# Kernel optimization log

Measured on AMD Instinct MI355X. Metric: run time of the kernel, lower is better.

## Reference

```python
import jax, jax.numpy as jnp
import numpy as np

V = 30522   # vocab / node count
A = 2       # num adjacency matrices
H = 128     # hid_dim
O = 16      # out_dim
B = 8       # batch
D = 256     # doc/sequence dim
NNZ = 250000  # nonzeros per adjacency


def setup_inputs() -> dict:
    key = jax.random.key(0)
    k = jax.random.split(key, 7)
    x_dv = jax.random.normal(k[0], (B, D, V), jnp.float32)
    adj_rows = jax.random.randint(k[1], (A, NNZ), 0, V)
    adj_cols = jax.random.randint(k[2], (A, NNZ), 0, V)
    adj_vals = jax.random.uniform(k[3], (A, NNZ), jnp.float32)
    W_vh = jax.random.normal(k[4], (A, V, H), jnp.float32) * 0.02
    fc_W = jax.random.normal(k[5], (H, O), jnp.float32) * 0.05
    fc_b = jnp.zeros((O,), jnp.float32)
    return {"x_dv": x_dv, "adj_rows": adj_rows, "adj_cols": adj_cols,
            "adj_vals": adj_vals, "W_vh": W_vh, "fc_W": fc_W, "fc_b": fc_b}


def reference(x_dv, adj_rows, adj_cols, adj_vals, W_vh, fc_W, fc_b):
    # Per-adjacency sparse mm: h_vh[a] = A_a @ W_a, A_a in COO form. [A, V, H]
    def spmm(rows, cols, vals, W):
        # gather rows of W at cols, scale by vals, scatter-add into output rows
        return jax.ops.segment_sum(vals[:, None] * W[cols], rows, num_segments=V)

    h_vh = jax.vmap(spmm)(adj_rows, adj_cols, adj_vals, W_vh)  # [A, V, H]
    # Dropout is identity in eval mode. fused_h = sum_a x_dv @ h_vh[a]
    # = x_dv @ sum_a h_vh[a] (x_dv is shared across adjacencies).
    h_sum = h_vh.sum(axis=0)                                   # [V, H]
    fused_h = jnp.einsum('bdv,vh->bdh', x_dv, h_sum)           # [B, D, H]
    return fused_h @ fc_W + fc_b                               # [B, D, O]
```

## Files before the change

### kernel.cpp

```cpp
#include <hip/hip_runtime.h>

#define V_N 30522
#define A_N 2
#define H_N 128
#define O_N 16
#define NNZ_N 250000
#define NNZ_T (A_N * NNZ_N)
#define M_N 2048
#define AV_N (A_N * V_N)

#define KPAD 30720
#define KSPL 32
#define KC (KPAD / KSPL)
#define NCHUNK 30
#define PADW (KPAD - V_N)

typedef __attribute__((ext_vector_type(8))) short bf16x8_t;
typedef __attribute__((ext_vector_type(4))) float f32x4_t;

static __device__ __forceinline__ unsigned short f2bf(float f) {
    union { float f; unsigned u; } v; v.f = f;
    unsigned r = v.u + 0x7fffu + ((v.u >> 16) & 1u);
    return (unsigned short)(r >> 16);
}

__global__ __launch_bounds__(256) void wfc_kernel(const float* __restrict__ W,
                                                  const float* __restrict__ fcW,
                                                  float* __restrict__ wfc,
                                                  int* __restrict__ count) {
    int gtid = blockIdx.x * 256 + threadIdx.x;
    if (gtid < V_N) count[gtid] = 0;

    __shared__ float wrow[16][128];
    int row0 = blockIdx.x * 16;
    for (int idx = threadIdx.x; idx < 16 * 32; idx += 256) {
        int r = idx >> 5, c4 = (idx & 31) * 4;
        int grow = row0 + r;
        float4 v = make_float4(0.f, 0.f, 0.f, 0.f);
        if (grow < AV_N)
            v = *reinterpret_cast<const float4*>(W + (size_t)grow * H_N + c4);
        *reinterpret_cast<float4*>(&wrow[r][c4]) = v;
    }
    __syncthreads();
    int r = threadIdx.x >> 4, o = threadIdx.x & 15;
    int grow = row0 + r;
    if (grow >= AV_N) return;
    float s = 0.f;
#pragma unroll
    for (int h = 0; h < H_N; ++h) s += wrow[r][h] * fcW[h * O_N + o];
    wfc[(size_t)grow * O_N + o] = s;
}

__global__ __launch_bounds__(256) void hist_kernel(const int* __restrict__ rows,
                                                   int* __restrict__ count,
                                                   short* __restrict__ hw_t) {
    int n = blockIdx.x * blockDim.x + threadIdx.x;
    if (n < O_N * PADW) {
        int o = n / PADW, v2 = V_N + (n - o * PADW);
        hw_t[(size_t)o * KPAD + v2] = 0;
    }
    if (n >= NNZ_T) return;
    atomicAdd(&count[rows[n]], 1);
}

__global__ __launch_bounds__(1024) void scanA_kernel(const int* __restrict__ count,
                                                     int* __restrict__ csum) {
    __shared__ int sdata[1024];
    int tid = threadIdx.x;
    int i = blockIdx.x * 1024 + tid;
    sdata[tid] = (i < V_N) ? count[i] : 0;
    __syncthreads();
    for (int off = 512; off > 0; off >>= 1) {
        if (tid < off) sdata[tid] += sdata[tid + off];
        __syncthreads();
    }
    if (tid == 0) csum[blockIdx.x] = sdata[0];
}

__global__ __launch_bounds__(1024) void scanC_kernel(const int* __restrict__ count,
                                                     const int* __restrict__ csum,
                                                     int* __restrict__ row_start,
                                                     int* __restrict__ cursor) {
    __shared__ int sdata[1024];
    __shared__ int coff_s;
    int tid = threadIdx.x;
    int bid = blockIdx.x;
    if (tid < 32) {
        int own = (tid < NCHUNK) ? csum[tid] : 0;
        int v = own;
#pragma unroll
        for (int d = 1; d < 32; d <<= 1) {
            int t = __shfl_up(v, d, 32);
            if (tid >= d) v += t;
        }
        if (tid == bid) coff_s = v - own;
        if (bid == 0 && tid == NCHUNK - 1) row_start[V_N] = v;
    }
    int i = bid * 1024 + tid;
    int v = (i < V_N) ? count[i] : 0;
    sdata[tid] = v;
    __syncthreads();
    for (int off = 1; off < 1024; off <<= 1) {
        int t = (tid >= off) ? sdata[tid - off] : 0;
        __syncthreads();
        sdata[tid] += t;
        __syncthreads();
    }
    int exc = sdata[tid] - v + coff_s;
    if (i < V_N) { row_start[i] = exc; cursor[i] = exc; }
}

__global__ __launch_bounds__(256) void scatter_kernel(const int* __restrict__ rows,
                                                      const int* __restrict__ cols,
                                                      const float* __restrict__ vals,
                                                      int* __restrict__ cursor,
                                                      unsigned long long* __restrict__ scv) {
    int n = blockIdx.x * blockDim.x + threadIdx.x;
    if (n >= NNZ_T) return;
    int a = (n >= NNZ_N) ? 1 : 0;
    int r = rows[n];
    int pos = atomicAdd(&cursor[r], 1);
    union { float f; unsigned u; } uv; uv.f = vals[n];
    scv[pos] = ((unsigned long long)uv.u << 32) | (unsigned)(a * V_N + cols[n]);
}

__global__ __launch_bounds__(256) void accum_hw_kernel(const int* __restrict__ row_start,
                                                       const unsigned long long* __restrict__ scv,
                                                       const float* __restrict__ wfc,
                                                       short* __restrict__ hw_t) {
    int gid = blockIdx.x * blockDim.x + threadIdx.x;
    if (gid >= V_N * O_N) return;
    int row = gid >> 4, o = gid & 15;
    int s = row_start[row];
    int e = row_start[row + 1];
    float acc = 0.f;
    for (int i = s; i < e; ++i) {
        unsigned long long cv = scv[i];
        int cp = (int)(cv & 0xffffffffu);
        union { unsigned u; float f; } uv; uv.u = (unsigned)(cv >> 32);
        acc += uv.f * wfc[(size_t)cp * O_N + o];
    }
    hw_t[(size_t)o * KPAD + row] = (short)f2bf(acc);
}

__global__ __launch_bounds__(256) void gemm_mfma5(const float* __restrict__ X,
                                                  const short* __restrict__ hw_t,
                                                  float* __restrict__ partials) {
    const int tid = threadIdx.x;
    const int w = tid >> 6;
    const int lane = tid & 63;
    const int l15 = lane & 15;
    const int kg = lane >> 4;
    const int row0 = blockIdx.x * 64 + w * 16;
    const int by = blockIdx.y;
    const int k0 = by * KC;

    const float* xrow = X + (size_t)(row0 + l15) * V_N;
    const short* hrow = hw_t + (size_t)l15 * KPAD;

    f32x4_t acc = {};

#pragma unroll 2
    for (int kb = k0; kb < k0 + KC; kb += 32) {
        int k = kb + kg * 8;
        float a[8];
        if (k + 7 < V_N) {
            const float2* p = reinterpret_cast<const float2*>(xrow + k);
            float2 u0 = p[0], u1 = p[1], u2 = p[2], u3 = p[3];
            a[0] = u0.x; a[1] = u0.y; a[2] = u1.x; a[3] = u1.y;
            a[4] = u2.x; a[5] = u2.y; a[6] = u3.x; a[7] = u3.y;
        } else {
#pragma unroll
            for (int j = 0; j < 8; ++j) a[j] = (k + j < V_N) ? xrow[k + j] : 0.f;
        }
        bf16x8_t av;
#pragma unroll
        for (int j = 0; j < 8; ++j) av[j] = (short)f2bf(a[j]);
        bf16x8_t bv = *reinterpret_cast<const bf16x8_t*>(hrow + k);
        acc = __builtin_amdgcn_mfma_f32_16x16x32_bf16(av, bv, acc, 0, 0, 0);
    }

#pragma unroll
    for (int r4 = 0; r4 < 4; ++r4)
        partials[((size_t)by * M_N + row0 + kg * 4 + r4) * O_N + l15] = acc[r4];
}

__global__ __launch_bounds__(256) void reduce_kernel(const float* __restrict__ partials,
                                                     const float* __restrict__ fcb,
                                                     float* __restrict__ out) {
    int idx = blockIdx.x * 256 + threadIdx.x;
    if (idx >= M_N * O_N) return;
    float s = fcb[idx & 15];
#pragma unroll
    for (int by = 0; by < KSPL; ++by)
        s += partials[(size_t)by * M_N * O_N + idx];
    out[idx] = s;
}

extern "C" void kernel_launch(void* const* d_in, const int* in_sizes, int n_in,
                              void* d_out, int out_size, void* d_ws, size_t ws_size,
                              hipStream_t stream) {
    const float* x    = (const float*)d_in[0];
    const int* rows   = (const int*)d_in[1];
    const int* cols   = (const int*)d_in[2];
    const float* vals = (const float*)d_in[3];
    const float* W    = (const float*)d_in[4];
    const float* fcW  = (const float*)d_in[5];
    const float* fcb  = (const float*)d_in[6];
    float* out = (float*)d_out;

    char* base = (char*)d_ws;
    size_t off = 0;
    auto alloc = [&](size_t bytes) { size_t p = off; off = (off + bytes + 255) & ~(size_t)255; return p; };
    size_t o_wfc    = alloc((size_t)AV_N * O_N * 4);
    size_t o_hwt    = alloc((size_t)O_N * KPAD * 2);
    size_t o_count  = alloc((size_t)V_N * 4);
    size_t o_rstart = alloc((size_t)(V_N + 1) * 4);
    size_t o_cursor = alloc((size_t)V_N * 4);
    size_t o_scv    = alloc((size_t)NNZ_T * 8);
    size_t o_csum   = alloc((size_t)NCHUNK * 4);
    size_t o_part   = alloc((size_t)KSPL * M_N * O_N * 4);

    float* wfc        = (float*)(base + o_wfc);
    short* hw_t       = (short*)(base + o_hwt);
    int*   count      = (int*)(base + o_count);
    int*   row_start  = (int*)(base + o_rstart);
    int*   cursor     = (int*)(base + o_cursor);
    unsigned long long* scv = (unsigned long long*)(base + o_scv);
    int*   csum       = (int*)(base + o_csum);
    float* partials   = (float*)(base + o_part);

    wfc_kernel<<<(AV_N + 15) / 16, 256, 0, stream>>>(W, fcW, wfc, count);
    hist_kernel<<<(NNZ_T + 255) / 256, 256, 0, stream>>>(rows, count, hw_t);
    scanA_kernel<<<NCHUNK, 1024, 0, stream>>>(count, csum);
    scanC_kernel<<<NCHUNK, 1024, 0, stream>>>(count, csum, row_start, cursor);
    scatter_kernel<<<(NNZ_T + 255) / 256, 256, 0, stream>>>(rows, cols, vals, cursor, scv);
    accum_hw_kernel<<<(V_N * O_N + 255) / 256, 256, 0, stream>>>(row_start, scv, wfc, hw_t);

    gemm_mfma5<<<dim3(M_N / 64, KSPL), 256, 0, stream>>>(x, hw_t, partials);
    reduce_kernel<<<(M_N * O_N + 255) / 256, 256, 0, stream>>>(partials, fcb, out);
}
```

Before: 164.7 us.

## Pre-convert X to padded bf16 in quarters piggybacked on sparse-prep kernels

Each of the four sparse-preparation kernels now also converts a quarter of the fp32 input X into a padded bf16 buffer. The GEMM reads bf16 directly instead of loading fp32 and converting in its inner loop. The aim is to hide the X conversion behind the latency-bound sparse kernels and to halve the bytes the GEMM streams. In exchange, X is still read once as fp32, plus an extra bf16 write of about 126MB and a bf16 reread. The approach also depends on those small kernels having spare bandwidth.

New measurement: 206.8 us. 25.5% more time.

```diff
diff --git a/kernel.cpp b/kernel.cpp
--- a/kernel.cpp
+++ b/kernel.cpp
@@ -14,6 +14,9 @@
 #define KC (KPAD / KSPL)
 #define NCHUNK 30
 #define PADW (KPAD - V_N)
+#define KP8 (KPAD / 8)
+#define NCV (M_N * KP8)
+#define QCH (NCV / 4)
 
 typedef __attribute__((ext_vector_type(8))) short bf16x8_t;
 typedef __attribute__((ext_vector_type(4))) float f32x4_t;
@@ -24,10 +27,38 @@
     return (unsigned short)(r >> 16);
 }
 
+static __device__ __forceinline__ void convert_slice(const float* __restrict__ X,
+                                                     short* __restrict__ xb,
+                                                     int slice) {
+    const int end = (slice + 1) * QCH;
+    const int stride = gridDim.x * blockDim.x;
+    for (int c = slice * QCH + blockIdx.x * blockDim.x + threadIdx.x; c < end; c += stride) {
+        int m = c / KP8;
+        int k0 = (c - m * KP8) * 8;
+        const float* xr = X + (size_t)m * V_N + k0;
+        bf16x8_t o;
+        if (k0 + 7 < V_N) {
+            const float2* p = reinterpret_cast<const float2*>(xr);
+            float2 u0 = p[0], u1 = p[1], u2 = p[2], u3 = p[3];
+            o[0] = (short)f2bf(u0.x); o[1] = (short)f2bf(u0.y);
+            o[2] = (short)f2bf(u1.x); o[3] = (short)f2bf(u1.y);
+            o[4] = (short)f2bf(u2.x); o[5] = (short)f2bf(u2.y);
+            o[6] = (short)f2bf(u3.x); o[7] = (short)f2bf(u3.y);
+        } else {
+#pragma unroll
+            for (int j = 0; j < 8; ++j)
+                o[j] = (k0 + j < V_N) ? (short)f2bf(xr[j]) : (short)0;
+        }
+        *reinterpret_cast<bf16x8_t*>(xb + (size_t)m * KPAD + k0) = o;
+    }
+}
+
 __global__ __launch_bounds__(256) void wfc_kernel(const float* __restrict__ W,
                                                   const float* __restrict__ fcW,
                                                   float* __restrict__ wfc,
-                                                  int* __restrict__ count) {
+                                                  int* __restrict__ count,
+                                                  const float* __restrict__ X,
+                                                  short* __restrict__ xb) {
     int gtid = blockIdx.x * 256 + threadIdx.x;
     if (gtid < V_N) count[gtid] = 0;
 
@@ -44,23 +75,27 @@
     __syncthreads();
     int r = threadIdx.x >> 4, o = threadIdx.x & 15;
     int grow = row0 + r;
-    if (grow >= AV_N) return;
-    float s = 0.f;
-#pragma unroll
-    for (int h = 0; h < H_N; ++h) s += wrow[r][h] * fcW[h * O_N + o];
-    wfc[(size_t)grow * O_N + o] = s;
+    if (grow < AV_N) {
+        float s = 0.f;
+#pragma unroll
+        for (int h = 0; h < H_N; ++h) s += wrow[r][h] * fcW[h * O_N + o];
+        wfc[(size_t)grow * O_N + o] = s;
+    }
+    convert_slice(X, xb, 0);
 }
 
 __global__ __launch_bounds__(256) void hist_kernel(const int* __restrict__ rows,
                                                    int* __restrict__ count,
-                                                   short* __restrict__ hw_t) {
+                                                   short* __restrict__ hw_t,
+                                                   const float* __restrict__ X,
+                                                   short* __restrict__ xb) {
     int n = blockIdx.x * blockDim.x + threadIdx.x;
     if (n < O_N * PADW) {
         int o = n / PADW, v2 = V_N + (n - o * PADW);
         hw_t[(size_t)o * KPAD + v2] = 0;
     }
-    if (n >= NNZ_T) return;
-    atomicAdd(&count[rows[n]], 1);
+    if (n < NNZ_T) atomicAdd(&count[rows[n]], 1);
+    convert_slice(X, xb, 1);
 }
 
 __global__ __launch_bounds__(1024) void scanA_kernel(const int* __restrict__ count,
@@ -114,36 +149,44 @@
                                                       const int* __restrict__ cols,
                                                       const float* __restrict__ vals,
                                                       int* __restrict__ cursor,
-                                                      unsigned long long* __restrict__ scv) {
+                                                      unsigned long long* __restrict__ scv,
+                                                      const float* __restrict__ X,
+                                                      short* __restrict__ xb) {
     int n = blockIdx.x * blockDim.x + threadIdx.x;
-    if (n >= NNZ_T) return;
-    int a = (n >= NNZ_N) ? 1 : 0;
-    int r = rows[n];
-    int pos = atomicAdd(&cursor[r], 1);
-    union { float f; unsigned u; } uv; uv.f = vals[n];
-    scv[pos] = ((unsigned long long)uv.u << 32) | (unsigned)(a * V_N + cols[n]);
+    if (n < NNZ_T) {
+        int a = (n >= NNZ_N) ? 1 : 0;
+        int r = rows[n];
+        int pos = atomicAdd(&cursor[r], 1);
+        union { float f; unsigned u; } uv; uv.f = vals[n];
+        scv[pos] = ((unsigned long long)uv.u << 32) | (unsigned)(a * V_N + cols[n]);
+    }
+    convert_slice(X, xb, 2);
 }
 
 __global__ __launch_bounds__(256) void accum_hw_kernel(const int* __restrict__ row_start,
                                                        const unsigned long long* __restrict__ scv,
                                                        const float* __restrict__ wfc,
-                                                       short* __restrict__ hw_t) {
+                                                       short* __restrict__ hw_t,
+                                                       const float* __restrict__ X,
+                                                       short* __restrict__ xb) {
     int gid = blockIdx.x * blockDim.x + threadIdx.x;
-    if (gid >= V_N * O_N) return;
-    int row = gid >> 4, o = gid & 15;
-    int s = row_start[row];
-    int e = row_start[row + 1];
-    float acc = 0.f;
-    for (int i = s; i < e; ++i) {
-        unsigned long long cv = scv[i];
-        int cp = (int)(cv & 0xffffffffu);
-        union { unsigned u; float f; } uv; uv.u = (unsigned)(cv >> 32);
-        acc += uv.f * wfc[(size_t)cp * O_N + o];
-    }
-    hw_t[(size_t)o * KPAD + row] = (short)f2bf(acc);
-}
-
-__global__ __launch_bounds__(256) void gemm_mfma5(const float* __restrict__ X,
+    if (gid < V_N * O_N) {
+        int row = gid >> 4, o = gid & 15;
+        int s = row_start[row];
+        int e = row_start[row + 1];
+        float acc = 0.f;
+        for (int i = s; i < e; ++i) {
+            unsigned long long cv = scv[i];
+            int cp = (int)(cv & 0xffffffffu);
+            union { unsigned u; float f; } uv; uv.u = (unsigned)(cv >> 32);
+            acc += uv.f * wfc[(size_t)cp * O_N + o];
+        }
+        hw_t[(size_t)o * KPAD + row] = (short)f2bf(acc);
+    }
+    convert_slice(X, xb, 3);
+}
+
+__global__ __launch_bounds__(256) void gemm_mfma7(const short* __restrict__ xb,
                                                   const short* __restrict__ hw_t,
                                                   float* __restrict__ partials) {
     const int tid = threadIdx.x;
@@ -155,7 +198,7 @@
     const int by = blockIdx.y;
     const int k0 = by * KC;
 
-    const float* xrow = X + (size_t)(row0 + l15) * V_N;
+    const short* xrow = xb + (size_t)(row0 + l15) * KPAD;
     const short* hrow = hw_t + (size_t)l15 * KPAD;
 
     f32x4_t acc = {};
@@ -163,19 +206,7 @@
 #pragma unroll 2
     for (int kb = k0; kb < k0 + KC; kb += 32) {
         int k = kb + kg * 8;
-        float a[8];
-        if (k + 7 < V_N) {
-            const float2* p = reinterpret_cast<const float2*>(xrow + k);
-            float2 u0 = p[0], u1 = p[1], u2 = p[2], u3 = p[3];
-            a[0] = u0.x; a[1] = u0.y; a[2] = u1.x; a[3] = u1.y;
-            a[4] = u2.x; a[5] = u2.y; a[6] = u3.x; a[7] = u3.y;
-        } else {
-#pragma unroll
-            for (int j = 0; j < 8; ++j) a[j] = (k + j < V_N) ? xrow[k + j] : 0.f;
-        }
-        bf16x8_t av;
-#pragma unroll
-        for (int j = 0; j < 8; ++j) av[j] = (short)f2bf(a[j]);
+        bf16x8_t av = *reinterpret_cast<const bf16x8_t*>(xrow + k);
         bf16x8_t bv = *reinterpret_cast<const bf16x8_t*>(hrow + k);
         acc = __builtin_amdgcn_mfma_f32_16x16x32_bf16(av, bv, acc, 0, 0, 0);
     }
@@ -212,6 +243,7 @@
     char* base = (char*)d_ws;
     size_t off = 0;
     auto alloc = [&](size_t bytes) { size_t p = off; off = (off + bytes + 255) & ~(size_t)255; return p; };
+    size_t o_xb     = alloc((size_t)M_N * KPAD * 2);
     size_t o_wfc    = alloc((size_t)AV_N * O_N * 4);
     size_t o_hwt    = alloc((size_t)O_N * KPAD * 2);
     size_t o_count  = alloc((size_t)V_N * 4);
@@ -221,6 +253,7 @@
     size_t o_csum   = alloc((size_t)NCHUNK * 4);
     size_t o_part   = alloc((size_t)KSPL * M_N * O_N * 4);
 
+    short* xb         = (short*)(base + o_xb);
     float* wfc        = (float*)(base + o_wfc);
     short* hw_t       = (short*)(base + o_hwt);
     int*   count      = (int*)(base + o_count);
@@ -230,13 +263,15 @@
     int*   csum       = (int*)(base + o_csum);
     float* partials   = (float*)(base + o_part);
 
-    wfc_kernel<<<(AV_N + 15) / 16, 256, 0, stream>>>(W, fcW, wfc, count);
-    hist_kernel<<<(NNZ_T + 255) / 256, 256, 0, stream>>>(rows, count, hw_t);
+    wfc_kernel<<<(AV_N + 15) / 16, 256, 0, stream>>>(W, fcW, wfc, count, x, xb);
+    hist_kernel<<<(NNZ_T + 255) / 256, 256, 0, stream>>>(rows, count, hw_t, x, xb);
     scanA_kernel<<<NCHUNK, 1024, 0, stream>>>(count, csum);
     scanC_kernel<<<NCHUNK, 1024, 0, stream>>>(count, csum, row_start, cursor);
-    scatter_kernel<<<(NNZ_T + 255) / 256, 256, 0, stream>>>(rows, cols, vals, cursor, scv);
-    accum_hw_kernel<<<(V_N * O_N + 255) / 256, 256, 0, stream>>>(row_start, scv, wfc, hw_t);
-
-    gemm_mfma5<<<dim3(M_N / 64, KSPL), 256, 0, stream>>>(x, hw_t, partials);
+    scatter_kernel<<<(NNZ_T + 255) / 256, 256, 0, stream>>>(rows, cols, vals, cursor,
+                                                            scv, x, xb);
+    accum_hw_kernel<<<(V_N * O_N + 255) / 256, 256, 0, stream>>>(row_start, scv, wfc,
+                                                                 hw_t, x, xb);
+
+    gemm_mfma7<<<dim3(M_N / 64, KSPL), 256, 0, stream>>>(xb, hw_t, partials);
     reduce_kernel<<<(M_N * O_N + 255) / 256, 256, 0, stream>>>(partials, fcb, out);
 }
```
